# Optimization experiments

Hardware: AMD Instinct MI355X
Metric: run time of the kernel (lower is better)

Reference implementation:

```python
import jax, jax.numpy as jnp
import numpy as np

NUM_HEADS = 16
MASKED_BIAS = -10000.0


def setup_inputs() -> dict:
    key = jax.random.key(0)
    k1, k2, k3 = jax.random.split(key, 3)
    B, S, D = 4, 2048, 1024
    return {
        "hidden_states": jax.random.normal(k1, (B, S, D), dtype=jnp.float32),
        "attention_mask": jnp.ones((B, S), dtype=jnp.float32),
        "w_attn": jax.random.normal(k2, (D, 3 * D), dtype=jnp.float32) * 0.02,
        "b_attn": jax.random.normal(k3, (3 * D,), dtype=jnp.float32) * 0.1,
    }


def reference(hidden_states, attention_mask, w_attn, b_attn):
    B, S, D = hidden_states.shape
    H = NUM_HEADS
    Dh = D // H
    # Conv1D: x @ W + b  -> [B, S, 3D]
    qkv = hidden_states @ w_attn + b_attn
    q, k, v = jnp.split(qkv, 3, axis=-1)

    def split_heads(t):  # [B,S,D] -> [B,H,S,Dh]
        return t.reshape(B, S, H, Dh).transpose(0, 2, 1, 3)

    q, k, v = split_heads(q), split_heads(k), split_heads(v)
    present = jnp.stack([k, v], axis=0)  # concat_key_value

    # process_mask: (1 - mask) * -10000, broadcast [B,1,1,S]
    add_mask = (1.0 - attention_mask)[:, None, None, :] * MASKED_BIAS

    qk = jnp.einsum("bhqd,bhkd->bhqk", q, k)
    norm_qk = qk * (1.0 / float(Dh) ** 0.5)
    causal = jnp.tril(jnp.ones((S, S), dtype=bool))[None, None]
    attn_weights = jnp.where(causal, norm_qk, jnp.asarray(MASKED_BIAS, norm_qk.dtype))
    attn_weights = attn_weights + add_mask
    probs = jax.nn.softmax(attn_weights, axis=-1)
    attn_output = jnp.einsum("bhqk,bhkd->bhqd", probs, v)
    # merge heads -> [B,S,D]
    attn_output = attn_output.transpose(0, 2, 1, 3).reshape(B, S, D)
    return attn_output, present
```

## Files before the change

### kernel.cpp

```cpp
#include <hip/hip_runtime.h>
#include <stdint.h>


#define B_SZ    4
#define S_LEN   2048
#define D_MODEL 1024
#define N3      3072
#define H_NUM   16
#define DH      64
#define M_TOT   8192

typedef __attribute__((ext_vector_type(8))) short short8;
typedef __attribute__((ext_vector_type(4))) short bf16x4;
typedef __attribute__((ext_vector_type(4))) float f32x4;

#define LOG2E      1.4426950408889634f
#define SCL2E      0.18033688011112042f
#define MASKB2     (-14426.9504f)

__device__ __forceinline__ unsigned short f2b(float f) {
  union { float f; unsigned int u; } x;
  x.f = f;
  unsigned int u = x.u;
  u += 0x7fffu + ((u >> 16) & 1u);
  return (unsigned short)(u >> 16);
}

__device__ __forceinline__ unsigned int cvt_pk_bf16(float lo, float hi) {
  unsigned int r;
  asm("v_cvt_pk_bf16_f32 %0, %1, %2" : "=v"(r) : "v"(lo), "v"(hi));
  return r;
}

__device__ __forceinline__ float exp2_fast(float x) {
#if __has_builtin(__builtin_amdgcn_exp2f)
  return __builtin_amdgcn_exp2f(x);
#else
  return __expf(x * 0.6931471805599453f);
#endif
}

__device__ __forceinline__ f32x4 mfma16(bf16x4 a, bf16x4 b, f32x4 c) {
#if __has_builtin(__builtin_amdgcn_mfma_f32_16x16x16bf16_1k)
  return __builtin_amdgcn_mfma_f32_16x16x16bf16_1k(a, b, c, 0, 0, 0);
#else
  asm("v_mfma_f32_16x16x16_bf16 %0, %1, %2, %0" : "+v"(c) : "v"(a), "v"(b));
  return c;
#endif
}

__device__ __forceinline__ void async16(const void* g, void* l) {
  __builtin_amdgcn_global_load_lds((const __attribute__((address_space(1))) void*)g,
                                   (__attribute__((address_space(3))) void*)l,
                                   16, 0, 0);
}

__global__ void k_convert_x(const float* __restrict__ X, unsigned short* __restrict__ Xb) {
  const int i = (blockIdx.x * 256 + threadIdx.x) * 4;
  const float4 v = *(const float4*)(X + i);
  ushort4 o;
  o.x = f2b(v.x); o.y = f2b(v.y); o.z = f2b(v.z); o.w = f2b(v.w);
  *(ushort4*)(Xb + i) = o;
}

__global__ void k_wt(const float* __restrict__ W, unsigned short* __restrict__ Wt) {
  __shared__ float tile[32][33];
  const int n0 = blockIdx.x * 32, k0 = blockIdx.y * 32;
  const int tx = threadIdx.x, ty = threadIdx.y;
  for (int i = 0; i < 32; i += 8)
    tile[ty + i][tx] = W[(size_t)(k0 + ty + i) * N3 + n0 + tx];
  __syncthreads();
  for (int i = 0; i < 32; i += 8)
    Wt[(size_t)(n0 + ty + i) * D_MODEL + k0 + tx] = f2b(tile[tx][ty + i]);
}

__global__ __launch_bounds__(256) void k_gemm_qkv(
    const unsigned short* __restrict__ Xb, const unsigned short* __restrict__ Wt,
    const float* __restrict__ bias,
    unsigned short* __restrict__ Qb, unsigned short* __restrict__ Kb,
    float* __restrict__ presK, float* __restrict__ presV) {
  __shared__ __align__(16) unsigned short SMEM[8192];
  unsigned short* As = SMEM;
  unsigned short* Bs = SMEM + 4096;
  const int t = threadIdx.x;
  const int lane = t & 63, wave = t >> 6;
  const int g = lane >> 4, c = lane & 15;
  const int m0 = blockIdx.y * 128, n0 = blockIdx.x * 128;
  const int wm = (wave >> 1) * 64, wn = (wave & 1) * 64;

  const f32x4 zero = {0.f, 0.f, 0.f, 0.f};
  f32x4 acc[4][4];
  for (int i = 0; i < 4; ++i)
    for (int j = 0; j < 4; ++j) acc[i][j] = zero;

  const int row_a = t >> 2;
  const int col_a = (t & 3) * 8;
  const unsigned short* gA = Xb + (size_t)(m0 + row_a) * D_MODEL + col_a;
  const unsigned short* gB = Wt + (size_t)(n0 + row_a) * D_MODEL + col_a;
  const int wbase = wave * 1024;

  for (int k0 = 0; k0 < D_MODEL; k0 += 32) {
    __syncthreads();
    async16(gA + k0,                (char*)As + wbase);
    async16(gA + k0 + 64 * D_MODEL, (char*)As + 4096 + wbase);
    async16(gB + k0,                (char*)Bs + wbase);
    async16(gB + k0 + 64 * D_MODEL, (char*)Bs + 4096 + wbase);
    __syncthreads();

    short8 af[4], bf[4];
    for (int mi = 0; mi < 4; ++mi)
      af[mi] = *(const short8*)(As + (wm + mi * 16 + c) * 32 + g * 8);
    for (int ni = 0; ni < 4; ++ni)
      bf[ni] = *(const short8*)(Bs + (wn + ni * 16 + c) * 32 + g * 8);
    for (int mi = 0; mi < 4; ++mi)
      for (int ni = 0; ni < 4; ++ni)
        acc[mi][ni] = __builtin_amdgcn_mfma_f32_16x16x32_bf16(af[mi], bf[ni], acc[mi][ni], 0, 0, 0);
  }

  __syncthreads();

  const int sec = (n0 + wn) >> 10;
  const int h = ((n0 + wn) & 1023) >> 6;
  unsigned short* slab = SMEM + wave * 1152;
  float bv[4];
  for (int ni = 0; ni < 4; ++ni) bv[ni] = bias[n0 + wn + ni * 16 + c];

  for (int mi = 0; mi < 4; ++mi) {
    const int mrow = m0 + wm + mi * 16;

    if (sec != 2) {
      for (int ni = 0; ni < 4; ++ni)
        for (int r = 0; r < 4; ++r)
          slab[(g * 4 + r) * 72 + ni * 16 + c] = f2b(acc[mi][ni][r] + bv[ni]);
      const short8 w0 = *(const short8*)(slab + c * 72 + g * 16);
      const short8 w1 = *(const short8*)(slab + c * 72 + g * 16 + 8);
      const int srow = mrow + c;
      const int b = srow >> 11, s = srow & 2047;
      unsigned short* dst = (sec == 0 ? Qb : Kb) +
          ((size_t)((b * H_NUM + h) * S_LEN + s)) * DH + g * 16;
      *(short8*)(dst) = w0;
      *(short8*)(dst + 8) = w1;
    }
    if (sec >= 1) {
      float* dstf = (sec == 1) ? presK : presV;
      for (int ni = 0; ni < 4; ++ni) {
        const int dh = ni * 16 + c;
        for (int r = 0; r < 4; ++r) {
          const int m = mrow + g * 4 + r;
          const int b = m >> 11, s = m & 2047;
          dstf[((size_t)((b * H_NUM + h) * S_LEN + s)) * DH + dh] =
              acc[mi][ni][r] + bv[ni];
        }
      }
    }
  }
}

__global__ __launch_bounds__(256) void k_vt(const float* __restrict__ presV,
                                            unsigned short* __restrict__ Vt) {
  __shared__ unsigned short tile[64 * 72];
  const int t = threadIdx.x;
  const int bh = blockIdx.y;
  const int s0 = blockIdx.x * 64;
  const int row = t >> 2;
  const int dh0 = (t & 3) * 16;
  const float* src = presV + ((size_t)bh * S_LEN + s0 + row) * DH + dh0;
  for (int i = 0; i < 4; ++i) {
    const float4 v = *(const float4*)(src + i * 4);
    const int dh = dh0 + i * 4;
    tile[(dh + 0) * 72 + row] = f2b(v.x);
    tile[(dh + 1) * 72 + row] = f2b(v.y);
    tile[(dh + 2) * 72 + row] = f2b(v.z);
    tile[(dh + 3) * 72 + row] = f2b(v.w);
  }
  __syncthreads();
  const int dh = t >> 2, sc0 = (t & 3) * 16;
  unsigned short* dst = Vt + ((size_t)bh * DH + dh) * S_LEN + s0 + sc0;
  short8 o0, o1;
  for (int i = 0; i < 8; ++i) {
    o0[i] = (short)tile[dh * 72 + sc0 + i];
    o1[i] = (short)tile[dh * 72 + sc0 + 8 + i];
  }
  *(short8*)(dst) = o0;
  *(short8*)(dst + 8) = o1;
}

__global__ __launch_bounds__(512) void k_flash(
    const unsigned short* __restrict__ Qb, const unsigned short* __restrict__ Kb,
    const unsigned short* __restrict__ Vt, const float* __restrict__ mask,
    float* __restrict__ out) {
  __shared__ __align__(16) unsigned short Ks[2][64 * 64];
  __shared__ __align__(16) unsigned short Vs[2][64 * 64];
  __shared__ __align__(16) float Ams[S_LEN];
  const int t = threadIdx.x;
  const int lane = t & 63, wave = t >> 6;
  const int g = lane >> 4, c = lane & 15;
  const int bh = blockIdx.y;
  const int b = bh >> 4, h = bh & 15;
  const int srow = t >> 3;
  const int schunk = (t & 7) ^ (srow & 7);
  const unsigned short* gK0 = Kb + ((size_t)bh * S_LEN + srow) * DH + schunk * 8;
  const unsigned short* gV0 = Vt + ((size_t)bh * DH + srow) * S_LEN + schunk * 8;
  const int kslot = c & 7;

  {
    const float4 mv = *(const float4*)(mask + (size_t)b * S_LEN + t * 4);
    float4 o;
    o.x = (1.0f - mv.x) * MASKB2;
    o.y = (1.0f - mv.y) * MASKB2;
    o.z = (1.0f - mv.z) * MASKB2;
    o.w = (1.0f - mv.w) * MASKB2;
    *(float4*)(Ams + t * 4) = o;
  }

  const f32x4 zero = {0.f, 0.f, 0.f, 0.f};

  for (int phase = 0; phase < 2; ++phase) {
    const int x = phase ? 15 - (int)blockIdx.x : (int)blockIdx.x;
    const int qb = x * 128;
    const int qw = qb + wave * 16;
    const int qrow = qw + c;

    short8 bq[2];
    const size_t qoff = ((size_t)bh * S_LEN + qw) * DH;
#pragma unroll
    for (int kc = 0; kc < 2; ++kc)
      bq[kc] = *(const short8*)(Qb + qoff + (size_t)c * DH + kc * 32 + g * 8);

    float m_i = -1e30f, l_i = 0.f;
    f32x4 o_acc[4];
#pragma unroll
    for (int dt = 0; dt < 4; ++dt) o_acc[dt] = zero;

    const int nt = (qb + 128) >> 6;
    async16(gK0, (char*)(&Ks[0][0]) + wave * 1024);
    async16(gV0, (char*)(&Vs[0][0]) + wave * 1024);

    for (int tt = 0; tt < nt; ++tt) {
      const int kb = tt << 6;
      const int cur = tt & 1;
      if (tt + 1 < nt) {
        async16(gK0 + (size_t)(kb + 64) * DH, (char*)(&Ks[cur ^ 1][0]) + wave * 1024);
        async16(gV0 + (kb + 64),              (char*)(&Vs[cur ^ 1][0]) + wave * 1024);
        asm volatile("s_waitcnt vmcnt(2) lgkmcnt(0)" ::: "memory");
      } else {
        asm volatile("s_waitcnt vmcnt(0) lgkmcnt(0)" ::: "memory");
      }
      __builtin_amdgcn_s_barrier();
      __builtin_amdgcn_sched_barrier(0);

      if (qw + 16 > kb) {
        const unsigned short* ks_base = &Ks[cur][0];
        const unsigned short* vs_base = &Vs[cur][0];

        f32x4 sc[4];
#pragma unroll
        for (int ks = 0; ks < 4; ++ks) {
          f32x4 a = zero;
          const int krow = ks * 16 + c;
#pragma unroll
          for (int kc = 0; kc < 2; ++kc) {
            const short8 ak = *(const short8*)(ks_base + krow * 64 + (((kc * 4 + g) ^ kslot) * 8));
            a = __builtin_amdgcn_mfma_f32_16x16x32_bf16(ak, bq[kc], a, 0, 0, 0);
          }
          sc[ks] = a;
        }

        const bool need_causal = (kb + 63 > qw);
        float mxk[4];
#pragma unroll
        for (int ks = 0; ks < 4; ++ks) {
          const float4 amv = *(const float4*)(Ams + kb + ks * 16 + g * 4);
          float am4[4];
          am4[0] = amv.x; am4[1] = amv.y; am4[2] = amv.z; am4[3] = amv.w;
#pragma unroll
          for (int r = 0; r < 4; ++r) {
            float v = sc[ks][r] * SCL2E + am4[r];
            if (need_causal && (kb + ks * 16 + g * 4 + r > qrow))
              v = MASKB2 + am4[r];
            sc[ks][r] = v;
          }
          mxk[ks] = fmaxf(fmaxf(sc[ks][0], sc[ks][1]), fmaxf(sc[ks][2], sc[ks][3]));
        }

        float mx = fmaxf(fmaxf(mxk[0], mxk[1]), fmaxf(mxk[2], mxk[3]));
        mx = fmaxf(mx, __shfl_xor(mx, 16));
        mx = fmaxf(mx, __shfl_xor(mx, 32));
        const float mnew = fmaxf(m_i, mx);
        const float alpha = exp2_fast(m_i - mnew);
        m_i = mnew;

        bf16x4 pk[4];
        float rsk[4];
#pragma unroll
        for (int ks = 0; ks < 4; ++ks) {
          const float p0 = exp2_fast(sc[ks][0] - mnew);
          const float p1 = exp2_fast(sc[ks][1] - mnew);
          const float p2 = exp2_fast(sc[ks][2] - mnew);
          const float p3 = exp2_fast(sc[ks][3] - mnew);
          rsk[ks] = (p0 + p1) + (p2 + p3);
          union { unsigned int u[2]; bf16x4 v4; } pu;
          pu.u[0] = cvt_pk_bf16(p0, p1);
          pu.u[1] = cvt_pk_bf16(p2, p3);
          pk[ks] = pu.v4;
        }
        float rs = (rsk[0] + rsk[1]) + (rsk[2] + rsk[3]);
        rs += __shfl_xor(rs, 16);
        rs += __shfl_xor(rs, 32);
        l_i = l_i * alpha + rs;
#pragma unroll
        for (int dt = 0; dt < 4; ++dt) o_acc[dt] *= alpha;

#pragma unroll
        for (int dt = 0; dt < 4; ++dt) {
          const int vrow = dt * 16 + c;
#pragma unroll
          for (int ks = 0; ks < 4; ++ks) {
            const bf16x4 av = *(const bf16x4*)(vs_base + vrow * 64 +
                (((2 * ks + (g >> 1)) ^ kslot) * 8) + (g & 1) * 4);
            o_acc[dt] = mfma16(av, pk[ks], o_acc[dt]);
          }
        }
      }
      __builtin_amdgcn_sched_barrier(0);
      __builtin_amdgcn_s_barrier();
    }

    const float inv = 1.0f / l_i;
    float* orow = out + ((size_t)(b * S_LEN + qrow)) * D_MODEL + h * DH;
#pragma unroll
    for (int dt = 0; dt < 4; ++dt) {
      float4 o;
      o.x = o_acc[dt][0] * inv;
      o.y = o_acc[dt][1] * inv;
      o.z = o_acc[dt][2] * inv;
      o.w = o_acc[dt][3] * inv;
      *(float4*)(orow + dt * 16 + g * 4) = o;
    }
  }
}

extern "C" void kernel_launch(void* const* d_in, const int* in_sizes, int n_in,
                              void* d_out, int out_size, void* d_ws, size_t ws_size,
                              hipStream_t stream) {
  const float* X    = (const float*)d_in[0];
  const float* mask = (const float*)d_in[1];
  const float* W    = (const float*)d_in[2];
  const float* bias = (const float*)d_in[3];

  float* out   = (float*)d_out;
  float* presK = out + (size_t)M_TOT * D_MODEL;
  float* presV = presK + (size_t)M_TOT * D_MODEL;

  char* ws = (char*)d_ws;
  unsigned short* Xb = (unsigned short*)(ws);
  unsigned short* Wt = (unsigned short*)(ws + 16777216);
  unsigned short* Qb = (unsigned short*)(ws + 23068672);
  unsigned short* Kb = (unsigned short*)(ws + 39845888);
  unsigned short* Vt = (unsigned short*)(ws + 56623104);

  k_convert_x<<<dim3(8192), dim3(256), 0, stream>>>(X, Xb);
  k_wt<<<dim3(96, 32), dim3(32, 8), 0, stream>>>(W, Wt);
  k_gemm_qkv<<<dim3(24, 64), dim3(256), 0, stream>>>(Xb, Wt, bias, Qb, Kb, presK, presV);
  k_vt<<<dim3(32, 64), dim3(256), 0, stream>>>(presV, Vt);
  k_flash<<<dim3(8, 64), dim3(512), 0, stream>>>(Qb, Kb, Vt, mask, out);
}
```

Baseline: 291.7 us.

## Permute V transpose layout for 128-bit LDS reads and skip small rescales

The V-transpose kernel now writes keys in a permuted order so that each lane in the PV MFMA loop loads its two k-slices with one 128-bit LDS read instead of two 64-bit reads. The online-softmax rescale of the accumulators and the running sum is now skipped when the new block's max is within a threshold of the running max. This is meant to cut LDS instruction count and per-iteration rescale multiplies. The lazy rescale lets unnormalised values grow by up to 2^8, which could affect bf16 precision of P, and the permutation must match the score layout exactly.

New measurement: 286.2 us. No clear change (-1.9%).

```diff
diff --git a/kernel.cpp b/kernel.cpp
--- a/kernel.cpp
+++ b/kernel.cpp
@@ -174,12 +174,15 @@
     tile[(dh + 3) * 72 + row] = f2b(v.w);
   }
   __syncthreads();
-  const int dh = t >> 2, sc0 = (t & 3) * 16;
-  unsigned short* dst = Vt + ((size_t)bh * DH + dh) * S_LEN + s0 + sc0;
+  const int dh = t >> 2, p0 = (t & 3) * 16;
+  unsigned short* dst = Vt + ((size_t)bh * DH + dh) * S_LEN + s0 + p0;
   short8 o0, o1;
   for (int i = 0; i < 8; ++i) {
-    o0[i] = (short)tile[dh * 72 + sc0 + i];
-    o1[i] = (short)tile[dh * 72 + sc0 + 8 + i];
+    const int pa = p0 + i, pb = p0 + 8 + i;
+    const int ka = (((pa >> 2) & 3) << 4) | (((pa >> 4) & 3) << 2) | (pa & 3);
+    const int kb = (((pb >> 2) & 3) << 4) | (((pb >> 4) & 3) << 2) | (pb & 3);
+    o0[i] = (short)tile[dh * 72 + ka];
+    o1[i] = (short)tile[dh * 72 + kb];
   }
   *(short8*)(dst) = o0;
   *(short8*)(dst + 8) = o1;
@@ -286,18 +289,23 @@
         float mx = fmaxf(fmaxf(mxk[0], mxk[1]), fmaxf(mxk[2], mxk[3]));
         mx = fmaxf(mx, __shfl_xor(mx, 16));
         mx = fmaxf(mx, __shfl_xor(mx, 32));
-        const float mnew = fmaxf(m_i, mx);
-        const float alpha = exp2_fast(m_i - mnew);
-        m_i = mnew;
+        if (!__all(mx <= m_i + 8.0f)) {
+          const float mnew = fmaxf(m_i, mx);
+          const float alpha = exp2_fast(m_i - mnew);
+          m_i = mnew;
+          l_i *= alpha;
+#pragma unroll
+          for (int dt = 0; dt < 4; ++dt) o_acc[dt] *= alpha;
+        }
 
         bf16x4 pk[4];
         float rsk[4];
 #pragma unroll
         for (int ks = 0; ks < 4; ++ks) {
-          const float p0 = exp2_fast(sc[ks][0] - mnew);
-          const float p1 = exp2_fast(sc[ks][1] - mnew);
-          const float p2 = exp2_fast(sc[ks][2] - mnew);
-          const float p3 = exp2_fast(sc[ks][3] - mnew);
+          const float p0 = exp2_fast(sc[ks][0] - m_i);
+          const float p1 = exp2_fast(sc[ks][1] - m_i);
+          const float p2 = exp2_fast(sc[ks][2] - m_i);
+          const float p3 = exp2_fast(sc[ks][3] - m_i);
           rsk[ks] = (p0 + p1) + (p2 + p3);
           union { unsigned int u[2]; bf16x4 v4; } pu;
           pu.u[0] = cvt_pk_bf16(p0, p1);
@@ -307,18 +315,17 @@
         float rs = (rsk[0] + rsk[1]) + (rsk[2] + rsk[3]);
         rs += __shfl_xor(rs, 16);
         rs += __shfl_xor(rs, 32);
-        l_i = l_i * alpha + rs;
-#pragma unroll
-        for (int dt = 0; dt < 4; ++dt) o_acc[dt] *= alpha;
+        l_i += rs;
 
 #pragma unroll
         for (int dt = 0; dt < 4; ++dt) {
           const int vrow = dt * 16 + c;
 #pragma unroll
-          for (int ks = 0; ks < 4; ++ks) {
-            const bf16x4 av = *(const bf16x4*)(vs_base + vrow * 64 +
-                (((2 * ks + (g >> 1)) ^ kslot) * 8) + (g & 1) * 4);
-            o_acc[dt] = mfma16(av, pk[ks], o_acc[dt]);
+          for (int jp = 0; jp < 2; ++jp) {
+            union { short8 s8; bf16x4 h[2]; } vv;
+            vv.s8 = *(const short8*)(vs_base + vrow * 64 + (((2 * g + jp) ^ kslot) * 8));
+            o_acc[dt] = mfma16(vv.h[0], pk[2 * jp], o_acc[dt]);
+            o_acc[dt] = mfma16(vv.h[1], pk[2 * jp + 1], o_acc[dt]);
           }
         }
       }
```
